# Kernel tuning notes

Measured on AMD Instinct MI355X. Metric: run time of the kernel, lower is better.

## Reference

```python
import math
import jax, jax.numpy as jnp
import numpy as np

DEGREE = 5
LN_EPS = 1e-5


def hermite_psi(C, r):
    # x_d = tanh(linspace(-1,1,C)) * (sqrt(2r+1)+1), shape [C]
    x_d = jnp.tanh(jnp.linspace(-1.0, 1.0, C)) * (math.sqrt(2 * r + 1) + 1.0)
    g = jnp.exp(-x_d ** 2 / 2.0)
    rows = [math.pi ** (-0.25) * g]
    if r > 0:
        rows.append(math.sqrt(2.0) * math.pi ** (-0.25) * x_d * g)
    for k in range(2, r + 1):
        rows.append(math.sqrt(2.0 / k) * x_d * rows[-1] - math.sqrt((k - 1) / k) * rows[-2])
    return jnp.stack(rows)  # [r+1, C]


def setup_inputs() -> dict:
    key = jax.random.key(0)
    k1, k2 = jax.random.split(key)
    B, C, H, W = 16, 512, 64, 64
    O = 512
    x = jax.random.normal(k1, (B, C, H, W), dtype=jnp.float32)
    ln_w = jnp.ones((C,), dtype=jnp.float32)
    ln_b = jnp.zeros((C,), dtype=jnp.float32)
    fc_w = jax.random.normal(k2, (O, C), dtype=jnp.float32) * (1.0 / math.sqrt(C))
    fc_b = jnp.zeros((O,), dtype=jnp.float32)
    return {"x": x, "ln_w": ln_w, "ln_b": ln_b, "fc_w": fc_w, "fc_b": fc_b}


def reference(x, ln_w, ln_b, fc_w, fc_b):
    B, C, H, W = x.shape
    O = fc_w.shape[0]
    # [B, HW, C]
    q = x.reshape(B, C, H * W).transpose(0, 2, 1)
    # LayerNorm over channels (biased variance, eps=1e-5)
    mu = q.mean(axis=-1, keepdims=True)
    var = ((q - mu) ** 2).mean(axis=-1, keepdims=True)
    q = (q - mu) / jnp.sqrt(var + LN_EPS) * ln_w + ln_b
    # Constant Hermite basis [r+1, C]
    psi = hermite_psi(C, DEGREE).astype(x.dtype)
    # Tiny cross-attention: scores [B, HW, r+1]
    scores = jnp.einsum('bnc,rc->bnr', q, psi) / math.sqrt(C)
    attn = jax.nn.softmax(scores, axis=-1)
    y = jnp.einsum('bnr,rc->bnc', attn, psi)  # [B, HW, C]
    # 1x1 conv == pointwise GEMM over channels
    out = jnp.einsum('bnc,oc->bon', y, fc_w) + fc_b[None, :, None]
    return out.reshape(B, O, H, W)
```

## Files before the change

### kernel.cpp

```cpp
#include <hip/hip_runtime.h>
#include <math.h>

#define C 512
#define NPIX 4096
#define BATCH 16
#define O 512
#define R 6
#define LN_EPS 1e-5f
#define ATTN_OFF 16384

typedef float vf4 __attribute__((ext_vector_type(4)));


__global__ __launch_bounds__(512) void setup_psi(const float* __restrict__ lnw,
                                                 const float* __restrict__ lnb,
                                                 float* __restrict__ ws) {
    __shared__ float sh_psi[R * C];
    const int c = threadIdx.x;
    float t = -1.0f + 2.0f * (float)c / 511.0f;
    float xd = tanhf(t) * 4.31662479035539984911f;
    float g = expf(-0.5f * xd * xd);
    const float pi_m14 = 0.75112554446494248286f;
    float rows[R];
    rows[0] = pi_m14 * g;
    rows[1] = 1.41421356237309504880f * pi_m14 * xd * g;
    #pragma unroll
    for (int k = 2; k <= 5; ++k)
        rows[k] = sqrtf(2.0f / k) * xd * rows[k - 1] - sqrtf((k - 1.0f) / k) * rows[k - 2];
    float w = lnw[c];
    #pragma unroll
    for (int r = 0; r < R; ++r) {
        sh_psi[r * C + c] = rows[r];
        ws[8192 + r * C + c] = rows[r];
        ws[c * 8 + r] = rows[r] * w;
    }
    __syncthreads();
    const int wv = threadIdx.x >> 6;
    const int l = threadIdx.x & 63;
    #pragma unroll
    for (int pass = 0; pass < 2; ++pass) {
        int combo = pass * 8 + wv;
        if (combo < 12) {
            int r = (combo < 6) ? combo : combo - 6;
            const float* vec = (combo < 6) ? lnw : lnb;
            float acc = 0.f;
            #pragma unroll
            for (int j = 0; j < 8; ++j) {
                int cc = l + 64 * j;
                acc += vec[cc] * sh_psi[r * C + cc];
            }
            #pragma unroll
            for (int m = 32; m >= 1; m >>= 1) acc += __shfl_xor(acc, m, 64);
            if (l == 0) ws[(combo < 6 ? 4096 : 4104) + r] = acc;
        }
    }
}

__global__ __launch_bounds__(64) void setup_M(const float* __restrict__ fcw,
                                              const float* __restrict__ fcb,
                                              float* __restrict__ ws) {
    const int o = blockIdx.x;
    const int lane = threadIdx.x;
    const float* psi = ws + 8192;
    float acc[R] = {0.f, 0.f, 0.f, 0.f, 0.f, 0.f};
    for (int c = lane; c < C; c += 64) {
        float w = fcw[o * C + c];
        #pragma unroll
        for (int r = 0; r < R; ++r) acc[r] += psi[r * C + c] * w;
    }
    #pragma unroll
    for (int r = 0; r < R; ++r)
        for (int m = 32; m >= 1; m >>= 1) acc[r] += __shfl_xor(acc[r], m, 64);
    if (lane == 0) {
        float bias = fcb[o];
        #pragma unroll
        for (int r = 0; r < R; ++r) ws[4112 + r * O + o] = acc[r] + bias;
    }
}

__global__ __launch_bounds__(512) void stats_kernel(const float* __restrict__ x,
                                                    const float* __restrict__ ws,
                                                    float* __restrict__ attn) {
    __shared__ float part[8][8][256];
    const int tid = threadIdx.x;
    const int wv = tid >> 6;
    const int l = tid & 63;
    const int b = blockIdx.x >> 4;
    const int pxg = blockIdx.x & 15;
    const int n0 = pxg << 8;
    const int wuni = __builtin_amdgcn_readfirstlane(wv);

    const float* xb = x + (((size_t)(b * C + (wuni << 6))) << 12) + n0 + (l << 2);
    const float* wbase = ws + ((size_t)(wuni << 6) << 3);

    float4 s = {0.f,0.f,0.f,0.f}, ss = s;
    float4 a0 = s, a1 = s, a2 = s, a3 = s, a4 = s, a5 = s;
    #pragma unroll 8
    for (int i = 0; i < 64; ++i) {
        float4 xv = *(const float4*)(xb + ((size_t)i << 12));
        const float* wr = wbase + (i << 3);
        float w0 = wr[0], w1 = wr[1], w2 = wr[2];
        float w3 = wr[3], w4 = wr[4], w5 = wr[5];
        s.x += xv.x;  s.y += xv.y;  s.z += xv.z;  s.w += xv.w;
        ss.x += xv.x * xv.x; ss.y += xv.y * xv.y; ss.z += xv.z * xv.z; ss.w += xv.w * xv.w;
        a0.x += xv.x * w0; a0.y += xv.y * w0; a0.z += xv.z * w0; a0.w += xv.w * w0;
        a1.x += xv.x * w1; a1.y += xv.y * w1; a1.z += xv.z * w1; a1.w += xv.w * w1;
        a2.x += xv.x * w2; a2.y += xv.y * w2; a2.z += xv.z * w2; a2.w += xv.w * w2;
        a3.x += xv.x * w3; a3.y += xv.y * w3; a3.z += xv.z * w3; a3.w += xv.w * w3;
        a4.x += xv.x * w4; a4.y += xv.y * w4; a4.z += xv.z * w4; a4.w += xv.w * w4;
        a5.x += xv.x * w5; a5.y += xv.y * w5; a5.z += xv.z * w5; a5.w += xv.w * w5;
    }
    *(float4*)&part[wv][0][l << 2] = s;
    *(float4*)&part[wv][1][l << 2] = ss;
    *(float4*)&part[wv][2][l << 2] = a0;
    *(float4*)&part[wv][3][l << 2] = a1;
    *(float4*)&part[wv][4][l << 2] = a2;
    *(float4*)&part[wv][5][l << 2] = a3;
    *(float4*)&part[wv][6][l << 2] = a4;
    *(float4*)&part[wv][7][l << 2] = a5;
    __syncthreads();

    if (tid < 256) {
        float v[8];
        #pragma unroll
        for (int st = 0; st < 8; ++st) {
            float acc = 0.f;
            #pragma unroll
            for (int w = 0; w < 8; ++w) acc += part[w][st][tid];
            v[st] = acc;
        }
        float mu = v[0] * (1.0f / 512.0f);
        float var = v[1] * (1.0f / 512.0f) - mu * mu;
        float rsig = rsqrtf(var + LN_EPS);
        const float invsq = 0.04419417382415922f;
        float sc[R], mx = -1e30f;
        #pragma unroll
        for (int r = 0; r < R; ++r) {
            float swp = ws[4096 + r], sbp = ws[4104 + r];
            sc[r] = ((v[2 + r] - mu * swp) * rsig + sbp) * invsq;
            mx = fmaxf(mx, sc[r]);
        }
        float es = 0.f, at[R];
        #pragma unroll
        for (int r = 0; r < R; ++r) { at[r] = expf(sc[r] - mx); es += at[r]; }
        float inv = 1.0f / es;
        #pragma unroll
        for (int r = 0; r < R; ++r)
            attn[(((size_t)(b * 6 + r)) << 12) + n0 + tid] = at[r] * inv;
    }
}

__global__ __launch_bounds__(256) void bcast_kernel(const float* __restrict__ ws,
                                                    float* __restrict__ out) {
    const int tid = threadIdx.x;
    const int bid = blockIdx.x;
    const int b = bid >> 8;
    const int pxg = (bid >> 6) & 3;
    const int og = bid & 63;
    const int n = (pxg << 10) + (tid << 2);

    const float* attn = ws + ATTN_OFF;
    float4 ar[R];
    #pragma unroll
    for (int r = 0; r < R; ++r)
        ar[r] = *(const float4*)(attn + (((size_t)(b * 6 + r)) << 12) + n);

    float* ob = out + (((size_t)(b * O + (og << 3))) << 12) + n;
    #pragma unroll
    for (int j = 0; j < 8; ++j) {
        int o = (og << 3) + j;
        float m0 = ws[4112 + 0 * O + o];
        float m1 = ws[4112 + 1 * O + o];
        float m2 = ws[4112 + 2 * O + o];
        float m3 = ws[4112 + 3 * O + o];
        float m4 = ws[4112 + 4 * O + o];
        float m5 = ws[4112 + 5 * O + o];
        vf4 res;
        res.x = ar[0].x * m0 + ar[1].x * m1 + ar[2].x * m2 + ar[3].x * m3 + ar[4].x * m4 + ar[5].x * m5;
        res.y = ar[0].y * m0 + ar[1].y * m1 + ar[2].y * m2 + ar[3].y * m3 + ar[4].y * m4 + ar[5].y * m5;
        res.z = ar[0].z * m0 + ar[1].z * m1 + ar[2].z * m2 + ar[3].z * m3 + ar[4].z * m4 + ar[5].z * m5;
        res.w = ar[0].w * m0 + ar[1].w * m1 + ar[2].w * m2 + ar[3].w * m3 + ar[4].w * m4 + ar[5].w * m5;
        __builtin_nontemporal_store(res, (vf4*)(ob + ((size_t)j << 12)));
    }
}

extern "C" void kernel_launch(void* const* d_in, const int* in_sizes, int n_in,
                              void* d_out, int out_size, void* d_ws, size_t ws_size,
                              hipStream_t stream) {
    const float* x    = (const float*)d_in[0];
    const float* ln_w = (const float*)d_in[1];
    const float* ln_b = (const float*)d_in[2];
    const float* fc_w = (const float*)d_in[3];
    const float* fc_b = (const float*)d_in[4];
    float* out = (float*)d_out;
    float* ws = (float*)d_ws;

    setup_psi<<<1, 512, 0, stream>>>(ln_w, ln_b, ws);
    setup_M<<<O, 64, 0, stream>>>(fc_w, fc_b, ws);
    stats_kernel<<<BATCH * 16, 512, 0, stream>>>(x, ws, ws + ATTN_OFF);
    bcast_kernel<<<4096, 256, 0, stream>>>(ws, out);
}
```

Baseline: 243.6 us.

## Fuse stats and broadcast kernels, merge setup kernels into one launch

Merges the two setup kernels into one launch: each block recomputes the Hermite rows locally, and one extra block handles the LayerNorm weight and bias projections. The stats and broadcast kernels are fused so attention weights stay in shared memory, which removes the global attn round trip and one launch. Pixel tiles shrink to 128 per block with 2-wide vectors, giving 512 blocks, and M is stored interleaved. The trade-off is narrower memory accesses: 8-byte loads and stores instead of 16-byte ones, and each block now writes all 512 output channels for its pixels.

```diff
diff --git a/kernel.cpp b/kernel.cpp
--- a/kernel.cpp
+++ b/kernel.cpp
@@ -7,120 +7,132 @@
 #define O 512
 #define R 6
 #define LN_EPS 1e-5f
-#define ATTN_OFF 16384
 
-typedef float vf4 __attribute__((ext_vector_type(4)));
+typedef float vf2 __attribute__((ext_vector_type(2)));
 
 
-__global__ __launch_bounds__(512) void setup_psi(const float* __restrict__ lnw,
-                                                 const float* __restrict__ lnb,
-                                                 float* __restrict__ ws) {
-    __shared__ float sh_psi[R * C];
-    const int c = threadIdx.x;
+__device__ __forceinline__ void hermite_rows(int c, float rows[R]) {
     float t = -1.0f + 2.0f * (float)c / 511.0f;
     float xd = tanhf(t) * 4.31662479035539984911f;
     float g = expf(-0.5f * xd * xd);
     const float pi_m14 = 0.75112554446494248286f;
-    float rows[R];
     rows[0] = pi_m14 * g;
     rows[1] = 1.41421356237309504880f * pi_m14 * xd * g;
     #pragma unroll
     for (int k = 2; k <= 5; ++k)
         rows[k] = sqrtf(2.0f / k) * xd * rows[k - 1] - sqrtf((k - 1.0f) / k) * rows[k - 2];
-    float w = lnw[c];
-    #pragma unroll
-    for (int r = 0; r < R; ++r) {
-        sh_psi[r * C + c] = rows[r];
-        ws[8192 + r * C + c] = rows[r];
-        ws[c * 8 + r] = rows[r] * w;
-    }
-    __syncthreads();
-    const int wv = threadIdx.x >> 6;
-    const int l = threadIdx.x & 63;
-    #pragma unroll
-    for (int pass = 0; pass < 2; ++pass) {
-        int combo = pass * 8 + wv;
-        if (combo < 12) {
-            int r = (combo < 6) ? combo : combo - 6;
-            const float* vec = (combo < 6) ? lnw : lnb;
-            float acc = 0.f;
+}
+
+__global__ __launch_bounds__(64) void setup_all(const float* __restrict__ lnw,
+                                                const float* __restrict__ lnb,
+                                                const float* __restrict__ fcw,
+                                                const float* __restrict__ fcb,
+                                                float* __restrict__ ws) {
+    const int o = blockIdx.x;
+    const int l = threadIdx.x;
+    if (o < O) {
+        float acc[R] = {0.f, 0.f, 0.f, 0.f, 0.f, 0.f};
+        #pragma unroll
+        for (int k = 0; k < 8; ++k) {
+            int c = l + (k << 6);
+            float rows[R];
+            hermite_rows(c, rows);
+            float w = fcw[o * C + c];
             #pragma unroll
-            for (int j = 0; j < 8; ++j) {
-                int cc = l + 64 * j;
-                acc += vec[cc] * sh_psi[r * C + cc];
+            for (int r = 0; r < R; ++r) acc[r] += rows[r] * w;
+        }
+        #pragma unroll
+        for (int r = 0; r < R; ++r)
+            #pragma unroll
+            for (int m = 32; m >= 1; m >>= 1) acc[r] += __shfl_xor(acc[r], m, 64);
+        if (l == 0) {
+            float bias = fcb[o];
+            float* M = ws + 4112 + o * 8;
+            #pragma unroll
+            for (int r = 0; r < R; ++r) M[r] = acc[r] + bias;
+        }
+    } else {
+        float sw[R] = {0.f, 0.f, 0.f, 0.f, 0.f, 0.f};
+        float sb[R] = {0.f, 0.f, 0.f, 0.f, 0.f, 0.f};
+        #pragma unroll
+        for (int k = 0; k < 8; ++k) {
+            int c = l + (k << 6);
+            float rows[R];
+            hermite_rows(c, rows);
+            float w = lnw[c], bb = lnb[c];
+            float* dst = ws + c * 8;
+            #pragma unroll
+            for (int r = 0; r < R; ++r) {
+                float rw = rows[r] * w;
+                dst[r] = rw;
+                sw[r] += rw;
+                sb[r] += rows[r] * bb;
             }
+        }
+        #pragma unroll
+        for (int r = 0; r < R; ++r) {
             #pragma unroll
-            for (int m = 32; m >= 1; m >>= 1) acc += __shfl_xor(acc, m, 64);
-            if (l == 0) ws[(combo < 6 ? 4096 : 4104) + r] = acc;
+            for (int m = 32; m >= 1; m >>= 1) {
+                sw[r] += __shfl_xor(sw[r], m, 64);
+                sb[r] += __shfl_xor(sb[r], m, 64);
+            }
+        }
+        if (l == 0) {
+            #pragma unroll
+            for (int r = 0; r < R; ++r) { ws[4096 + r] = sw[r]; ws[4104 + r] = sb[r]; }
         }
     }
 }
 
-__global__ __launch_bounds__(64) void setup_M(const float* __restrict__ fcw,
-                                              const float* __restrict__ fcb,
-                                              float* __restrict__ ws) {
-    const int o = blockIdx.x;
-    const int lane = threadIdx.x;
-    const float* psi = ws + 8192;
-    float acc[R] = {0.f, 0.f, 0.f, 0.f, 0.f, 0.f};
-    for (int c = lane; c < C; c += 64) {
-        float w = fcw[o * C + c];
-        #pragma unroll
-        for (int r = 0; r < R; ++r) acc[r] += psi[r * C + c] * w;
-    }
-    #pragma unroll
-    for (int r = 0; r < R; ++r)
-        for (int m = 32; m >= 1; m >>= 1) acc[r] += __shfl_xor(acc[r], m, 64);
-    if (lane == 0) {
-        float bias = fcb[o];
-        #pragma unroll
-        for (int r = 0; r < R; ++r) ws[4112 + r * O + o] = acc[r] + bias;
-    }
-}
-
-__global__ __launch_bounds__(512) void stats_kernel(const float* __restrict__ x,
+__global__ __launch_bounds__(512) void fused_kernel(const float* __restrict__ x,
                                                     const float* __restrict__ ws,
-                                                    float* __restrict__ attn) {
-    __shared__ float part[8][8][256];
+                                                    float* __restrict__ out) {
+    __shared__ float part[8][8][128];
+    __shared__ float attn_s[R][128];
     const int tid = threadIdx.x;
     const int wv = tid >> 6;
     const int l = tid & 63;
-    const int b = blockIdx.x >> 4;
-    const int pxg = blockIdx.x & 15;
-    const int n0 = pxg << 8;
+    const int b = blockIdx.x >> 5;
+    const int pxg = blockIdx.x & 31;
+    const int n0 = pxg << 7;
+    const int p2 = l << 1;
     const int wuni = __builtin_amdgcn_readfirstlane(wv);
 
-    const float* xb = x + (((size_t)(b * C + (wuni << 6))) << 12) + n0 + (l << 2);
+    const float* xb = x + (((size_t)(b * C + (wuni << 6))) << 12) + n0 + p2;
     const float* wbase = ws + ((size_t)(wuni << 6) << 3);
 
-    float4 s = {0.f,0.f,0.f,0.f}, ss = s;
-    float4 a0 = s, a1 = s, a2 = s, a3 = s, a4 = s, a5 = s;
+    float sx = 0.f, sy = 0.f, ssx = 0.f, ssy = 0.f;
+    float a0x = 0.f, a0y = 0.f, a1x = 0.f, a1y = 0.f, a2x = 0.f, a2y = 0.f;
+    float a3x = 0.f, a3y = 0.f, a4x = 0.f, a4y = 0.f, a5x = 0.f, a5y = 0.f;
     #pragma unroll 8
     for (int i = 0; i < 64; ++i) {
-        float4 xv = *(const float4*)(xb + ((size_t)i << 12));
+        vf2 xv = *(const vf2*)(xb + ((size_t)i << 12));
         const float* wr = wbase + (i << 3);
         float w0 = wr[0], w1 = wr[1], w2 = wr[2];
         float w3 = wr[3], w4 = wr[4], w5 = wr[5];
-        s.x += xv.x;  s.y += xv.y;  s.z += xv.z;  s.w += xv.w;
-        ss.x += xv.x * xv.x; ss.y += xv.y * xv.y; ss.z += xv.z * xv.z; ss.w += xv.w * xv.w;
-        a0.x += xv.x * w0; a0.y += xv.y * w0; a0.z += xv.z * w0; a0.w += xv.w * w0;
-        a1.x += xv.x * w1; a1.y += xv.y * w1; a1.z += xv.z * w1; a1.w += xv.w * w1;
-        a2.x += xv.x * w2; a2.y += xv.y * w2; a2.z += xv.z * w2; a2.w += xv.w * w2;
-        a3.x += xv.x * w3; a3.y += xv.y * w3; a3.z += xv.z * w3; a3.w += xv.w * w3;
-        a4.x += xv.x * w4; a4.y += xv.y * w4; a4.z += xv.z * w4; a4.w += xv.w * w4;
-        a5.x += xv.x * w5; a5.y += xv.y * w5; a5.z += xv.z * w5; a5.w += xv.w * w5;
+        sx += xv.x;          sy += xv.y;
+        ssx += xv.x * xv.x;  ssy += xv.y * xv.y;
+        a0x += xv.x * w0;    a0y += xv.y * w0;
+        a1x += xv.x * w1;    a1y += xv.y * w1;
+        a2x += xv.x * w2;    a2y += xv.y * w2;
+        a3x += xv.x * w3;    a3y += xv.y * w3;
+        a4x += xv.x * w4;    a4y += xv.y * w4;
+        a5x += xv.x * w5;    a5y += xv.y * w5;
     }
-    *(float4*)&part[wv][0][l << 2] = s;
-    *(float4*)&part[wv][1][l << 2] = ss;
-    *(float4*)&part[wv][2][l << 2] = a0;
-    *(float4*)&part[wv][3][l << 2] = a1;
-    *(float4*)&part[wv][4][l << 2] = a2;
-    *(float4*)&part[wv][5][l << 2] = a3;
-    *(float4*)&part[wv][6][l << 2] = a4;
-    *(float4*)&part[wv][7][l << 2] = a5;
+    {
+        vf2 t;
+        t.x = sx;  t.y = sy;  *(vf2*)&part[wv][0][p2] = t;
+        t.x = ssx; t.y = ssy; *(vf2*)&part[wv][1][p2] = t;
+        t.x = a0x; t.y = a0y; *(vf2*)&part[wv][2][p2] = t;
+        t.x = a1x; t.y = a1y; *(vf2*)&part[wv][3][p2] = t;
+        t.x = a2x; t.y = a2y; *(vf2*)&part[wv][4][p2] = t;
+        t.x = a3x; t.y = a3y; *(vf2*)&part[wv][5][p2] = t;
+        t.x = a4x; t.y = a4y; *(vf2*)&part[wv][6][p2] = t;
+        t.x = a5x; t.y = a5y; *(vf2*)&part[wv][7][p2] = t;
+    }
     __syncthreads();
 
-    if (tid < 256) {
+    if (tid < 128) {
         float v[8];
         #pragma unroll
         for (int st = 0; st < 8; ++st) {
@@ -145,42 +157,29 @@
         for (int r = 0; r < R; ++r) { at[r] = expf(sc[r] - mx); es += at[r]; }
         float inv = 1.0f / es;
         #pragma unroll
-        for (int r = 0; r < R; ++r)
-            attn[(((size_t)(b * 6 + r)) << 12) + n0 + tid] = at[r] * inv;
+        for (int r = 0; r < R; ++r) attn_s[r][tid] = at[r] * inv;
     }
-}
+    __syncthreads();
 
-__global__ __launch_bounds__(256) void bcast_kernel(const float* __restrict__ ws,
-                                                    float* __restrict__ out) {
-    const int tid = threadIdx.x;
-    const int bid = blockIdx.x;
-    const int b = bid >> 8;
-    const int pxg = (bid >> 6) & 3;
-    const int og = bid & 63;
-    const int n = (pxg << 10) + (tid << 2);
-
-    const float* attn = ws + ATTN_OFF;
-    float4 ar[R];
+    float arx[R], ary[R];
     #pragma unroll
-    for (int r = 0; r < R; ++r)
-        ar[r] = *(const float4*)(attn + (((size_t)(b * 6 + r)) << 12) + n);
-
-    float* ob = out + (((size_t)(b * O + (og << 3))) << 12) + n;
-    #pragma unroll
-    for (int j = 0; j < 8; ++j) {
-        int o = (og << 3) + j;
-        float m0 = ws[4112 + 0 * O + o];
-        float m1 = ws[4112 + 1 * O + o];
-        float m2 = ws[4112 + 2 * O + o];
-        float m3 = ws[4112 + 3 * O + o];
-        float m4 = ws[4112 + 4 * O + o];
-        float m5 = ws[4112 + 5 * O + o];
-        vf4 res;
-        res.x = ar[0].x * m0 + ar[1].x * m1 + ar[2].x * m2 + ar[3].x * m3 + ar[4].x * m4 + ar[5].x * m5;
-        res.y = ar[0].y * m0 + ar[1].y * m1 + ar[2].y * m2 + ar[3].y * m3 + ar[4].y * m4 + ar[5].y * m5;
-        res.z = ar[0].z * m0 + ar[1].z * m1 + ar[2].z * m2 + ar[3].z * m3 + ar[4].z * m4 + ar[5].z * m5;
-        res.w = ar[0].w * m0 + ar[1].w * m1 + ar[2].w * m2 + ar[3].w * m3 + ar[4].w * m4 + ar[5].w * m5;
-        __builtin_nontemporal_store(res, (vf4*)(ob + ((size_t)j << 12)));
+    for (int r = 0; r < R; ++r) {
+        vf2 a = *(const vf2*)&attn_s[r][p2];
+        arx[r] = a.x; ary[r] = a.y;
+    }
+    const float* Ms = ws + 4112 + ((size_t)(wuni << 6) << 3);
+    float* ob = out + (((size_t)(b * O + (wuni << 6))) << 12) + n0 + p2;
+    #pragma unroll 8
+    for (int j = 0; j < 64; ++j) {
+        const float* mo = Ms + (j << 3);
+        float m0 = mo[0], m1 = mo[1], m2 = mo[2];
+        float m3 = mo[3], m4 = mo[4], m5 = mo[5];
+        vf2 res;
+        res.x = arx[0] * m0 + arx[1] * m1 + arx[2] * m2
+              + arx[3] * m3 + arx[4] * m4 + arx[5] * m5;
+        res.y = ary[0] * m0 + ary[1] * m1 + ary[2] * m2
+              + ary[3] * m3 + ary[4] * m4 + ary[5] * m5;
+        __builtin_nontemporal_store(res, (vf2*)(ob + ((size_t)j << 12)));
     }
 }
 
@@ -195,8 +194,6 @@
     float* out = (float*)d_out;
     float* ws = (float*)d_ws;
 
-    setup_psi<<<1, 512, 0, stream>>>(ln_w, ln_b, ws);
-    setup_M<<<O, 64, 0, stream>>>(fc_w, fc_b, ws);
-    stats_kernel<<<BATCH * 16, 512, 0, stream>>>(x, ws, ws + ATTN_OFF);
-    bcast_kernel<<<4096, 256, 0, stream>>>(ws, out);
+    setup_all<<<O + 1, 64, 0, stream>>>(ln_w, ln_b, fc_w, fc_b, ws);
+    fused_kernel<<<BATCH * 32, 512, 0, stream>>>(x, ws, out);
 }
```

Result: no change. 245.0 us (+0.6%).
